# Kernel optimization log

Measured on AMD Instinct MI355X. Metric: run time of the kernel, lower is better.

Reference implementation:

```python
import jax, jax.numpy as jnp
import numpy as np

STEPS = [1, 2, 3, 4, 5]
B, N, D, H = 16, 512, 512, 8
S = len(STEPS) + 1           # identity + one stack per step
FFN_HID = 2 * S              # ffn_hidden_multiplier = 2


def setup_inputs() -> dict:
    key = jax.random.key(0)
    ks = jax.random.split(key, 12)
    h = jax.random.normal(ks[0], (B, N, D), dtype=jnp.float32)
    adj = jax.random.uniform(ks[1], (B, N, N), dtype=jnp.float32)
    mask = jax.random.randint(ks[2], (B, N), 0, 2).astype(bool)
    mask = mask.at[:, 0].set(True)  # guarantee >=1 valid node per graph
    sd = 1.0 / np.sqrt(D)
    in_proj_w = jax.random.normal(ks[3], (3 * D, D), dtype=jnp.float32) * sd
    in_proj_b = jnp.zeros((3 * D,), dtype=jnp.float32)
    out_w = jax.random.normal(ks[4], (D, D), dtype=jnp.float32) * sd
    out_b = jnp.zeros((D,), dtype=jnp.float32)
    ffn_w1 = jax.random.normal(ks[5], (S, FFN_HID), dtype=jnp.float32) * (1.0 / np.sqrt(S))
    ffn_b1 = jnp.zeros((FFN_HID,), dtype=jnp.float32)
    ffn_w2 = jax.random.normal(ks[6], (FFN_HID, H), dtype=jnp.float32) * (1.0 / np.sqrt(FFN_HID))
    ffn_b2 = jnp.zeros((H,), dtype=jnp.float32)
    return dict(h=h, adj=adj, mask=mask,
                in_proj_w=in_proj_w, in_proj_b=in_proj_b,
                out_w=out_w, out_b=out_b,
                ffn_w1=ffn_w1, ffn_b1=ffn_b1, ffn_w2=ffn_w2, ffn_b2=ffn_b2)


def _adj_stack(adj, mask):
    # Mask invalid node pairs, row-normalize to a transition matrix P,
    # then stack [I, P^s for s in STEPS] -> [B, S, N, N].
    pair_mask = mask[:, :, None] & mask[:, None, :]
    A = jnp.where(pair_mask, adj, 0.0)
    rs = A.sum(-1, keepdims=True)
    P = A / jnp.where(rs == 0.0, 1.0, rs)
    eye = jnp.broadcast_to(jnp.eye(N, dtype=adj.dtype), (adj.shape[0], N, N))
    stacks = [eye]
    pw = eye
    for step in range(1, max(STEPS) + 1):
        pw = pw @ P
        if step in STEPS:
            stacks.append(pw)
    return jnp.stack(stacks, axis=1)  # [B, S, N, N]


def reference(h, adj, mask, in_proj_w, in_proj_b, out_w, out_b,
              ffn_w1, ffn_b1, ffn_w2, ffn_b2):
    hd = D // H
    stacks = _adj_stack(adj, mask)                      # [B,S,N,N]
    # per-pair edge FFN: [B,N,N,S] -> relu -> [B,N,N,H] -> [B,H,N,N]
    edge_in = stacks.transpose(0, 2, 3, 1)
    bias = jax.nn.relu(edge_in @ ffn_w1 + ffn_b1) @ ffn_w2 + ffn_b2
    bias = bias.transpose(0, 3, 1, 2)                   # [B,H,N,N]

    qkv = h @ in_proj_w.T + in_proj_b                   # [B,N,3D]
    q, k, v = jnp.split(qkv, 3, axis=-1)
    q = q.reshape(B, N, H, hd).transpose(0, 2, 1, 3)    # [B,H,N,hd]
    k = k.reshape(B, N, H, hd).transpose(0, 2, 1, 3)
    v = v.reshape(B, N, H, hd).transpose(0, 2, 1, 3)

    scores = jnp.einsum('bhqd,bhkd->bhqk', q, k) / np.sqrt(hd) + bias
    scores = jnp.where(mask[:, None, None, :], scores, -1e9)  # key padding
    attn = jax.nn.softmax(scores, axis=-1)              # [B,H,N,N]

    ctx = jnp.einsum('bhqk,bhkd->bhqd', attn, v)
    ctx = ctx.transpose(0, 2, 1, 3).reshape(B, N, D)
    atten_out = ctx @ out_w.T + out_b                   # [B,N,D]
    atten_weights = attn.mean(axis=1)                   # [B,N,N], head-avg as in torch MHA
    return atten_out, atten_weights
```

## Files before the change

### kernel.cpp

```cpp
#include <hip/hip_runtime.h>
#include <hip/hip_bf16.h>

#define Bz 16
#define Nn 512
#define Dd 512
#define Hh 8
#define HD 64

static const long NNl  = (long)Nn * Nn;
static const long BNNl = (long)Bz * Nn * Nn;

__device__ inline float bf2f(unsigned short u) {
    unsigned int x = ((unsigned int)u) << 16;
    return __uint_as_float(x);
}
__device__ inline unsigned short f2bf(float f) {
    __hip_bfloat16 h = __float2bfloat16(f);
    return *reinterpret_cast<unsigned short*>(&h);
}

__global__ __launch_bounds__(64)
void computeP(const float* __restrict__ adj, const int* __restrict__ mask,
              float* __restrict__ P)
{
    const int i = blockIdx.x;
    const int b = blockIdx.y;
    const int lane = threadIdx.x;
    const float* arow = adj + ((long)b * Nn + i) * Nn;
    const int*   mrow = mask + (long)b * Nn;
    const bool mi = (mrow[i] != 0);

    float vals[8];
    float s = 0.f;
    #pragma unroll
    for (int t = 0; t < 2; ++t) {
        const int c = lane * 4 + t * 256;
        float4 a4 = *(const float4*)&arow[c];
        int4   m4 = *(const int4*)&mrow[c];
        float v0 = (mi && m4.x) ? a4.x : 0.f;
        float v1 = (mi && m4.y) ? a4.y : 0.f;
        float v2 = (mi && m4.z) ? a4.z : 0.f;
        float v3 = (mi && m4.w) ? a4.w : 0.f;
        vals[t*4+0] = v0; vals[t*4+1] = v1; vals[t*4+2] = v2; vals[t*4+3] = v3;
        s += v0 + v1 + v2 + v3;
    }
    #pragma unroll
    for (int o = 1; o < 64; o <<= 1) s += __shfl_xor(s, o);
    const float den = (s == 0.f) ? 1.f : s;

    float* prow = P + ((long)b * Nn + i) * Nn;
    #pragma unroll
    for (int t = 0; t < 2; ++t) {
        const int c = lane * 4 + t * 256;
        float4 o4;
        o4.x = vals[t*4+0] / den;
        o4.y = vals[t*4+1] / den;
        o4.z = vals[t*4+2] / den;
        o4.w = vals[t*4+3] / den;
        *(float4*)&prow[c] = o4;
    }
}

template<bool BT, bool BIAS>
__global__ __launch_bounds__(256)
void gemm128(const float* __restrict__ A, const float* __restrict__ Bm,
             const float* __restrict__ bias, float* __restrict__ C,
             int M, int N, int K, long sA, long sB, long sC)
{
    __shared__ float As[16][128];
    __shared__ float Bs[16][128];

    const int bz = blockIdx.z;
    A  += (long)bz * sA;
    Bm += (long)bz * sB;
    C  += (long)bz * sC;
    const int bm = blockIdx.y * 128;
    const int bn = blockIdx.x * 128;
    const int tid = threadIdx.x;
    const int tx = tid & 15;
    const int ty = tid >> 4;

    float acc[8][8];
    #pragma unroll
    for (int i = 0; i < 8; ++i)
        #pragma unroll
        for (int j = 0; j < 8; ++j) acc[i][j] = 0.f;

    for (int k0 = 0; k0 < K; k0 += 16) {
        #pragma unroll
        for (int i = 0; i < 2; ++i) {
            const int r = (tid >> 2) + i * 64;
            const int c = (tid & 3) * 4;
            float4 a4 = *(const float4*)&A[(long)(bm + r) * K + k0 + c];
            As[c+0][r] = a4.x; As[c+1][r] = a4.y;
            As[c+2][r] = a4.z; As[c+3][r] = a4.w;
        }
        if (!BT) {
            #pragma unroll
            for (int i = 0; i < 2; ++i) {
                const int kk = (tid >> 5) + i * 8;
                const int c  = (tid & 31) * 4;
                *(float4*)&Bs[kk][c] =
                    *(const float4*)&Bm[(long)(k0 + kk) * N + bn + c];
            }
        } else {
            #pragma unroll
            for (int i = 0; i < 2; ++i) {
                const int cc = (tid >> 2) + i * 64;
                const int kk = (tid & 3) * 4;
                float4 b4 = *(const float4*)&Bm[(long)(bn + cc) * K + k0 + kk];
                Bs[kk+0][cc] = b4.x; Bs[kk+1][cc] = b4.y;
                Bs[kk+2][cc] = b4.z; Bs[kk+3][cc] = b4.w;
            }
        }
        __syncthreads();

        #pragma unroll
        for (int kk = 0; kk < 16; ++kk) {
            float a[8], bb[8];
            *(float4*)&a[0]  = *(const float4*)&As[kk][ty*4];
            *(float4*)&a[4]  = *(const float4*)&As[kk][64 + ty*4];
            *(float4*)&bb[0] = *(const float4*)&Bs[kk][tx*4];
            *(float4*)&bb[4] = *(const float4*)&Bs[kk][64 + tx*4];
            #pragma unroll
            for (int i = 0; i < 8; ++i)
                #pragma unroll
                for (int j = 0; j < 8; ++j)
                    acc[i][j] = fmaf(a[i], bb[j], acc[i][j]);
        }
        __syncthreads();
    }

    float bv[8];
    if (BIAS) {
        *(float4*)&bv[0] = *(const float4*)&bias[bn + tx*4];
        *(float4*)&bv[4] = *(const float4*)&bias[bn + 64 + tx*4];
    }
    #pragma unroll
    for (int i = 0; i < 8; ++i) {
        const int r = bm + ((i < 4) ? (ty*4 + i) : (64 + ty*4 + (i - 4)));
        float o0[4], o1[4];
        #pragma unroll
        for (int j = 0; j < 4; ++j) {
            o0[j] = acc[i][j]     + (BIAS ? bv[j]     : 0.f);
            o1[j] = acc[i][j + 4] + (BIAS ? bv[j + 4] : 0.f);
        }
        *(float4*)&C[(long)r * N + bn + tx*4]      = *(float4*)o0;
        *(float4*)&C[(long)r * N + bn + 64 + tx*4] = *(float4*)o1;
    }
}

template<bool BT, bool BIAS>
__global__ __launch_bounds__(256)
void gemm64(const float* __restrict__ A, const float* __restrict__ Bm,
            const float* __restrict__ bias, float* __restrict__ C,
            int M, int N, int K, long sA, long sB, long sC)
{
    __shared__ float As[16][128];
    __shared__ float Bs[16][64];

    const int bz = blockIdx.z;
    A  += (long)bz * sA;
    Bm += (long)bz * sB;
    C  += (long)bz * sC;
    const int bm = blockIdx.y * 128;
    const int bn = blockIdx.x * 64;
    const int tid = threadIdx.x;
    const int tx = tid & 15;
    const int ty = tid >> 4;

    float acc[8][4];
    #pragma unroll
    for (int i = 0; i < 8; ++i)
        #pragma unroll
        for (int j = 0; j < 4; ++j) acc[i][j] = 0.f;

    for (int k0 = 0; k0 < K; k0 += 16) {
        #pragma unroll
        for (int i = 0; i < 2; ++i) {
            const int r = (tid >> 2) + i * 64;
            const int c = (tid & 3) * 4;
            float4 a4 = *(const float4*)&A[(long)(bm + r) * K + k0 + c];
            As[c+0][r] = a4.x; As[c+1][r] = a4.y;
            As[c+2][r] = a4.z; As[c+3][r] = a4.w;
        }
        if (!BT) {
            const int kk = tid >> 4;
            const int c  = (tid & 15) * 4;
            *(float4*)&Bs[kk][c] =
                *(const float4*)&Bm[(long)(k0 + kk) * N + bn + c];
        } else {
            const int cc = tid >> 2;
            const int kk = (tid & 3) * 4;
            float4 b4 = *(const float4*)&Bm[(long)(bn + cc) * K + k0 + kk];
            Bs[kk+0][cc] = b4.x; Bs[kk+1][cc] = b4.y;
            Bs[kk+2][cc] = b4.z; Bs[kk+3][cc] = b4.w;
        }
        __syncthreads();

        #pragma unroll
        for (int kk = 0; kk < 16; ++kk) {
            float a[8], bb[4];
            *(float4*)&a[0]  = *(const float4*)&As[kk][ty*4];
            *(float4*)&a[4]  = *(const float4*)&As[kk][64 + ty*4];
            *(float4*)&bb[0] = *(const float4*)&Bs[kk][tx*4];
            #pragma unroll
            for (int i = 0; i < 8; ++i)
                #pragma unroll
                for (int j = 0; j < 4; ++j)
                    acc[i][j] = fmaf(a[i], bb[j], acc[i][j]);
        }
        __syncthreads();
    }

    float bv[4];
    if (BIAS) *(float4*)&bv[0] = *(const float4*)&bias[bn + tx*4];
    #pragma unroll
    for (int i = 0; i < 8; ++i) {
        const int r = bm + ((i < 4) ? (ty*4 + i) : (64 + ty*4 + (i - 4)));
        float o0[4];
        #pragma unroll
        for (int j = 0; j < 4; ++j)
            o0[j] = acc[i][j] + (BIAS ? bv[j] : 0.f);
        *(float4*)&C[(long)r * N + bn + tx*4] = *(float4*)o0;
    }
}

template<bool BF16OUT>
__global__ __launch_bounds__(256)
void bias_ffn(const float* __restrict__ powers,
              const float* __restrict__ w1, const float* __restrict__ b1,
              const float* __restrict__ w2, const float* __restrict__ b2,
              void* __restrict__ biasOut)
{
    __shared__ float sw1[6][12], sb1[12], sw2[12][8], sb2[8];
    const int tid = threadIdx.x;
    if (tid < 72)        sw1[tid/12][tid%12] = w1[tid];
    else if (tid < 84)   sb1[tid-72] = b1[tid-72];
    else if (tid < 180)  sw2[(tid-84)/8][(tid-84)%8] = w2[tid-84];
    else if (tid < 188)  sb2[tid-180] = b2[tid-180];
    __syncthreads();

    const int b = blockIdx.y;
    const int ql = tid >> 7;
    const int qrow = blockIdx.x * 2 + ql;
    const int kk = (tid & 127) * 4;

    float xp[5][4];
    #pragma unroll
    for (int s = 0; s < 5; ++s) {
        float4 t = *(const float4*)&powers[((long)(s*Bz+b))*NNl + (long)qrow*Nn + kk];
        xp[s][0]=t.x; xp[s][1]=t.y; xp[s][2]=t.z; xp[s][3]=t.w;
    }
    float outh[8][4];
    #pragma unroll
    for (int j = 0; j < 4; ++j) {
        float hid[12];
        #pragma unroll
        for (int jj = 0; jj < 12; ++jj) {
            float v = sb1[jj];
            if (qrow == kk + j) v += sw1[0][jj];
            v = fmaf(xp[0][j], sw1[1][jj], v);
            v = fmaf(xp[1][j], sw1[2][jj], v);
            v = fmaf(xp[2][j], sw1[3][jj], v);
            v = fmaf(xp[3][j], sw1[4][jj], v);
            v = fmaf(xp[4][j], sw1[5][jj], v);
            hid[jj] = fmaxf(v, 0.f);
        }
        #pragma unroll
        for (int h = 0; h < 8; ++h) {
            float a = sb2[h];
            #pragma unroll
            for (int jj = 0; jj < 12; ++jj) a = fmaf(hid[jj], sw2[jj][h], a);
            outh[h][j] = a;
        }
    }
    #pragma unroll
    for (int h = 0; h < 8; ++h) {
        const long off = ((long)(b*Hh+h))*NNl + (long)qrow*Nn + kk;
        if (BF16OUT) {
            ushort4 u;
            u.x = f2bf(outh[h][0]); u.y = f2bf(outh[h][1]);
            u.z = f2bf(outh[h][2]); u.w = f2bf(outh[h][3]);
            *(ushort4*)((unsigned short*)biasOut + off) = u;
        } else {
            float4 o = {outh[h][0], outh[h][1], outh[h][2], outh[h][3]};
            *(float4*)((float*)biasOut + off) = o;
        }
    }
}

__device__ inline int kswz(int row, int slot) {
    return row * 68 + (((slot ^ ((row >> 2) & 7)) & 15) << 2);
}

template<bool BF16B>
__global__ __launch_bounds__(256)
void attn2(const float* __restrict__ qkv, const void* __restrict__ biasT,
           const int* __restrict__ mask,
           float* __restrict__ ctx, float* __restrict__ wout)
{
    __shared__ float scT[512][17];
    __shared__ float kvs[64 * 68];

    const int qt = blockIdx.x, b = blockIdx.y;
    const int q0 = qt * 16;
    const int tid = threadIdx.x;

    const int qi = tid >> 4;
    const int kg = tid & 15;
    const int kq = tid >> 6;
    const int qg = (tid >> 4) & 3;
    const int dg = tid & 15;

    float wacc[32];
    #pragma unroll
    for (int i = 0; i < 32; ++i) wacc[i] = 0.f;

    for (int h = 0; h < Hh; ++h) {
        float4 qreg[16];
        {
            const float* qp = qkv + ((long)b*Nn + q0 + qi)*(3*Dd) + h*HD;
            #pragma unroll
            for (int t = 0; t < 16; ++t) qreg[t] = *(const float4*)&qp[t*4];
        }

        for (int kt = 0; kt < 8; ++kt) {
            {
                const int row = tid >> 2;
                const int sb  = (tid & 3) * 4;
                const float* kp = qkv + ((long)b*Nn + kt*64 + row)*(3*Dd)
                                  + Dd + h*HD + sb*4;
                #pragma unroll
                for (int t = 0; t < 4; ++t)
                    *(float4*)&kvs[kswz(row, sb + t)] = *(const float4*)&kp[t*4];
            }
            __syncthreads();

            const int kbase = kt*64 + kg*4;
            const int4 m4 = *(const int4*)&mask[(long)b*Nn + kbase];
            float bias4[4];
            if (BF16B) {
                ushort4 u = *(const ushort4*)((const unsigned short*)biasT
                            + ((long)(b*Hh+h))*NNl + (long)(q0+qi)*Nn + kbase);
                bias4[0] = bf2f(u.x); bias4[1] = bf2f(u.y);
                bias4[2] = bf2f(u.z); bias4[3] = bf2f(u.w);
            } else {
                float4 f = *(const float4*)((const float*)biasT
                            + ((long)(b*Hh+h))*NNl + (long)(q0+qi)*Nn + kbase);
                bias4[0]=f.x; bias4[1]=f.y; bias4[2]=f.z; bias4[3]=f.w;
            }
            const int mm[4] = {m4.x, m4.y, m4.z, m4.w};
            #pragma unroll
            for (int j = 0; j < 4; ++j) {
                const int krow = kg*4 + j;
                float s = 0.f;
                #pragma unroll
                for (int d4 = 0; d4 < 16; ++d4) {
                    float4 k4 = *(const float4*)&kvs[kswz(krow, d4)];
                    s += qreg[d4].x*k4.x + qreg[d4].y*k4.y
                       + qreg[d4].z*k4.z + qreg[d4].w*k4.w;
                }
                float sv = s * 0.125f + bias4[j];
                if (!mm[j]) sv = -1e9f;
                scT[kbase + j][qi] = sv;
            }
            __syncthreads();
        }

        {
            const int c = kg;
            float pv[32];
            float mx = -INFINITY;
            #pragma unroll
            for (int i = 0; i < 32; ++i) {
                pv[i] = scT[c + 16*i][qi];
                mx = fmaxf(mx, pv[i]);
            }
            #pragma unroll
            for (int o = 1; o < 16; o <<= 1) mx = fmaxf(mx, __shfl_xor(mx, o));
            float sum = 0.f;
            #pragma unroll
            for (int i = 0; i < 32; ++i) { pv[i] = expf(pv[i] - mx); sum += pv[i]; }
            #pragma unroll
            for (int o = 1; o < 16; o <<= 1) sum += __shfl_xor(sum, o);
            const float inv = 1.f / sum;
            #pragma unroll
            for (int i = 0; i < 32; ++i) {
                const float p = pv[i] * inv;
                scT[c + 16*i][qi] = p;
                wacc[i] += p;
            }
        }
        __syncthreads();

        float4 acc[4];
        #pragma unroll
        for (int i = 0; i < 4; ++i) acc[i] = make_float4(0.f, 0.f, 0.f, 0.f);

        for (int kt = 0; kt < 8; ++kt) {
            {
                const int row = tid >> 2;
                const int sb  = (tid & 3) * 4;
                const float* vp = qkv + ((long)b*Nn + kt*64 + row)*(3*Dd)
                                  + 2*Dd + h*HD + sb*4;
                #pragma unroll
                for (int t = 0; t < 4; ++t)
                    *(float4*)&kvs[kswz(row, sb + t)] = *(const float4*)&vp[t*4];
            }
            __syncthreads();

            #pragma unroll
            for (int kk2 = 0; kk2 < 16; ++kk2) {
                const int kl = kq*16 + kk2;
                const int k  = kt*64 + kl;
                float p0 = scT[k][qg*4+0];
                float p1 = scT[k][qg*4+1];
                float p2 = scT[k][qg*4+2];
                float p3 = scT[k][qg*4+3];
                float4 v4 = *(const float4*)&kvs[kswz(kl, dg)];
                acc[0].x = fmaf(p0, v4.x, acc[0].x); acc[0].y = fmaf(p0, v4.y, acc[0].y);
                acc[0].z = fmaf(p0, v4.z, acc[0].z); acc[0].w = fmaf(p0, v4.w, acc[0].w);
                acc[1].x = fmaf(p1, v4.x, acc[1].x); acc[1].y = fmaf(p1, v4.y, acc[1].y);
                acc[1].z = fmaf(p1, v4.z, acc[1].z); acc[1].w = fmaf(p1, v4.w, acc[1].w);
                acc[2].x = fmaf(p2, v4.x, acc[2].x); acc[2].y = fmaf(p2, v4.y, acc[2].y);
                acc[2].z = fmaf(p2, v4.z, acc[2].z); acc[2].w = fmaf(p2, v4.w, acc[2].w);
                acc[3].x = fmaf(p3, v4.x, acc[3].x); acc[3].y = fmaf(p3, v4.y, acc[3].y);
                acc[3].z = fmaf(p3, v4.z, acc[3].z); acc[3].w = fmaf(p3, v4.w, acc[3].w);
            }
            __syncthreads();
        }

        if (kq > 0) {
            float* dst = &kvs[0] + ((long)(kq-1)*64 + (qg*16 + dg)) * 16;
            #pragma unroll
            for (int i = 0; i < 4; ++i) *(float4*)&dst[i*4] = acc[i];
        }
        __syncthreads();
        if (kq == 0) {
            #pragma unroll
            for (int k2 = 0; k2 < 3; ++k2) {
                const float* src = &kvs[0] + ((long)k2*64 + (qg*16 + dg)) * 16;
                #pragma unroll
                for (int i = 0; i < 4; ++i) {
                    float4 t = *(const float4*)&src[i*4];
                    acc[i].x += t.x; acc[i].y += t.y; acc[i].z += t.z; acc[i].w += t.w;
                }
            }
            #pragma unroll
            for (int i = 0; i < 4; ++i)
                *(float4*)&ctx[((long)b*Nn + q0 + qg*4 + i)*Dd + h*HD + dg*4] = acc[i];
        }
        __syncthreads();
    }

    {
        float* wrow = wout + ((long)b*Nn + q0 + qi) * Nn;
        #pragma unroll
        for (int i = 0; i < 32; ++i) wrow[kg + 16*i] = wacc[i] * 0.125f;
    }
}

extern "C" void kernel_launch(void* const* d_in, const int* in_sizes, int n_in,
                              void* d_out, int out_size, void* d_ws, size_t ws_size,
                              hipStream_t stream)
{
    const float* h_in      = (const float*)d_in[0];
    const float* adj       = (const float*)d_in[1];
    const int*   mask      = (const int*)d_in[2];
    const float* in_proj_w = (const float*)d_in[3];
    const float* in_proj_b = (const float*)d_in[4];
    const float* out_w     = (const float*)d_in[5];
    const float* out_b     = (const float*)d_in[6];
    const float* ffn_w1    = (const float*)d_in[7];
    const float* ffn_b1    = (const float*)d_in[8];
    const float* ffn_w2    = (const float*)d_in[9];
    const float* ffn_b2    = (const float*)d_in[10];

    float* ws = (float*)d_ws;

    float* powers = ws;
    float* qkv    = ws;
    float* ctxb   = ws + 12582912;
    void*  biasT  = (void*)((char*)d_ws + 83886080);

    const bool fp32bias = (ws_size >= 218103808ull);

    float* out_atten = (float*)d_out;
    float* out_wts   = out_atten + BNNl;

    computeP<<<dim3(Nn, Bz), 64, 0, stream>>>(adj, mask, powers);

    for (int s = 1; s < 5; ++s) {
        gemm64<false, false><<<dim3(8, 4, Bz), 256, 0, stream>>>(
            powers + (long)(s-1)*BNNl, powers, nullptr, powers + (long)s*BNNl,
            Nn, Nn, Nn, NNl, NNl, NNl);
    }

    if (fp32bias)
        bias_ffn<false><<<dim3(Nn/2, Bz), 256, 0, stream>>>(
            powers, ffn_w1, ffn_b1, ffn_w2, ffn_b2, biasT);
    else
        bias_ffn<true><<<dim3(Nn/2, Bz), 256, 0, stream>>>(
            powers, ffn_w1, ffn_b1, ffn_w2, ffn_b2, biasT);

    gemm128<true, true><<<dim3(12, 4, Bz), 256, 0, stream>>>(
        h_in, in_proj_w, in_proj_b, qkv,
        Nn, 3*Dd, Dd, (long)Nn*Dd, 0, (long)Nn*3*Dd);

    if (fp32bias)
        attn2<false><<<dim3(Nn/16, Bz), 256, 0, stream>>>(qkv, biasT, mask, ctxb, out_wts);
    else
        attn2<true><<<dim3(Nn/16, Bz), 256, 0, stream>>>(qkv, biasT, mask, ctxb, out_wts);

    gemm64<true, true><<<dim3(8, 4, Bz), 256, 0, stream>>>(
        ctxb, out_w, out_b, out_atten,
        Nn, Dd, Dd, (long)Nn*Dd, 0, (long)Nn*Dd);
}
```

Before: 961.2 us.

## Register-block two query rows per thread and stage 128-key tiles in attn2

The score phase now has each thread compute scores for two query rows against one key. This reuses every K vector read from shared memory twice, and 128 keys are staged per synchronisation instead of 64, so there are fewer barriers. The score buffer stride is padded to 20 so the P·V loop can read four probabilities with one float4 load, and the launch bounds request two blocks per CU. The costs are more registers (two 16-float4 query sets) and double the K/V shared memory. The reduction scratch stride of 17 makes its float4 LDS accesses misaligned, which could split or misbehave.

```diff
diff --git a/kernel.cpp b/kernel.cpp
--- a/kernel.cpp
+++ b/kernel.cpp
@@ -295,18 +295,23 @@
 }
 
 template<bool BF16B>
-__global__ __launch_bounds__(256)
+__global__ __launch_bounds__(256, 2)
 void attn2(const float* __restrict__ qkv, const void* __restrict__ biasT,
            const int* __restrict__ mask,
            float* __restrict__ ctx, float* __restrict__ wout)
 {
-    __shared__ float scT[512][17];
-    __shared__ float kvs[64 * 68];
+    __shared__ float scTf[512 * 20];
+    __shared__ float kvs[2 * 4352];
 
     const int qt = blockIdx.x, b = blockIdx.y;
     const int q0 = qt * 16;
     const int tid = threadIdx.x;
 
+    const int w     = tid >> 6;
+    const int lane  = tid & 63;
+    const int tsel  = w >> 1;
+    const int qbase = 8 * (w & 1) + 2 * (lane >> 4);
+    const int kgq   = lane & 15;
     const int qi = tid >> 4;
     const int kg = tid & 15;
     const int kq = tid >> 6;
@@ -318,63 +323,68 @@
     for (int i = 0; i < 32; ++i) wacc[i] = 0.f;
 
     for (int h = 0; h < Hh; ++h) {
-        float4 qreg[16];
         {
-            const float* qp = qkv + ((long)b*Nn + q0 + qi)*(3*Dd) + h*HD;
-            #pragma unroll
-            for (int t = 0; t < 16; ++t) qreg[t] = *(const float4*)&qp[t*4];
-        }
-
-        for (int kt = 0; kt < 8; ++kt) {
-            {
-                const int row = tid >> 2;
-                const int sb  = (tid & 3) * 4;
-                const float* kp = qkv + ((long)b*Nn + kt*64 + row)*(3*Dd)
-                                  + Dd + h*HD + sb*4;
+            float4 qA[16], qB[16];
+            const float* qp0 = qkv + ((long)b*Nn + q0 + qbase)*(3*Dd) + h*HD;
+            const float* qp1 = qp0 + 3*Dd;
+            #pragma unroll
+            for (int t = 0; t < 16; ++t) {
+                qA[t] = *(const float4*)&qp0[t*4];
+                qB[t] = *(const float4*)&qp1[t*4];
+            }
+
+            for (int p = 0; p < 4; ++p) {
+                {
+                    const int row  = tid >> 1;
+                    const int half = tid & 1;
+                    const float* kp = qkv + ((long)b*Nn + p*128 + row)*(3*Dd)
+                                      + Dd + h*HD + half*32;
+                    float* base = &kvs[(row >> 6) * 4352];
+                    const int rIT = row & 63;
+                    #pragma unroll
+                    for (int t = 0; t < 8; ++t)
+                        *(float4*)&base[kswz(rIT, half*8 + t)] = *(const float4*)&kp[t*4];
+                }
+                __syncthreads();
+
                 #pragma unroll
-                for (int t = 0; t < 4; ++t)
-                    *(float4*)&kvs[kswz(row, sb + t)] = *(const float4*)&kp[t*4];
-            }
-            __syncthreads();
-
-            const int kbase = kt*64 + kg*4;
-            const int4 m4 = *(const int4*)&mask[(long)b*Nn + kbase];
-            float bias4[4];
-            if (BF16B) {
-                ushort4 u = *(const ushort4*)((const unsigned short*)biasT
-                            + ((long)(b*Hh+h))*NNl + (long)(q0+qi)*Nn + kbase);
-                bias4[0] = bf2f(u.x); bias4[1] = bf2f(u.y);
-                bias4[2] = bf2f(u.z); bias4[3] = bf2f(u.w);
-            } else {
-                float4 f = *(const float4*)((const float*)biasT
-                            + ((long)(b*Hh+h))*NNl + (long)(q0+qi)*Nn + kbase);
-                bias4[0]=f.x; bias4[1]=f.y; bias4[2]=f.z; bias4[3]=f.w;
-            }
-            const int mm[4] = {m4.x, m4.y, m4.z, m4.w};
-            #pragma unroll
-            for (int j = 0; j < 4; ++j) {
-                const int krow = kg*4 + j;
-                float s = 0.f;
-                #pragma unroll
-                for (int d4 = 0; d4 < 16; ++d4) {
-                    float4 k4 = *(const float4*)&kvs[kswz(krow, d4)];
-                    s += qreg[d4].x*k4.x + qreg[d4].y*k4.y
-                       + qreg[d4].z*k4.z + qreg[d4].w*k4.w;
+                for (int j = 0; j < 4; ++j) {
+                    const int rowIT = kgq + 16*j;
+                    const float* tb = &kvs[tsel * 4352];
+                    float s0 = 0.f, s1 = 0.f;
+                    #pragma unroll
+                    for (int d4 = 0; d4 < 16; ++d4) {
+                        float4 k4 = *(const float4*)&tb[kswz(rowIT, d4)];
+                        s0 += qA[d4].x*k4.x + qA[d4].y*k4.y + qA[d4].z*k4.z + qA[d4].w*k4.w;
+                        s1 += qB[d4].x*k4.x + qB[d4].y*k4.y + qB[d4].z*k4.z + qB[d4].w*k4.w;
+                    }
+                    const int gkey = p*128 + tsel*64 + rowIT;
+                    float b0, b1;
+                    if (BF16B) {
+                        const unsigned short* bp = (const unsigned short*)biasT
+                            + ((long)(b*Hh+h))*NNl + (long)(q0+qbase)*Nn + gkey;
+                        b0 = bf2f(bp[0]); b1 = bf2f(bp[Nn]);
+                    } else {
+                        const float* bp = (const float*)biasT
+                            + ((long)(b*Hh+h))*NNl + (long)(q0+qbase)*Nn + gkey;
+                        b0 = bp[0]; b1 = bp[Nn];
+                    }
+                    const int mv = mask[(long)b*Nn + gkey];
+                    float v0 = s0 * 0.125f + b0;
+                    float v1 = s1 * 0.125f + b1;
+                    if (!mv) { v0 = -1e9f; v1 = -1e9f; }
+                    *(float2*)&scTf[gkey*20 + qbase] = make_float2(v0, v1);
                 }
-                float sv = s * 0.125f + bias4[j];
-                if (!mm[j]) sv = -1e9f;
-                scT[kbase + j][qi] = sv;
-            }
-            __syncthreads();
+                __syncthreads();
+            }
         }
 
         {
-            const int c = kg;
             float pv[32];
             float mx = -INFINITY;
             #pragma unroll
             for (int i = 0; i < 32; ++i) {
-                pv[i] = scT[c + 16*i][qi];
+                pv[i] = scTf[(kg + 16*i)*20 + qi];
                 mx = fmaxf(mx, pv[i]);
             }
             #pragma unroll
@@ -388,7 +398,7 @@
             #pragma unroll
             for (int i = 0; i < 32; ++i) {
                 const float p = pv[i] * inv;
-                scT[c + 16*i][qi] = p;
+                scTf[(kg + 16*i)*20 + qi] = p;
                 wacc[i] += p;
             }
         }
@@ -398,41 +408,45 @@
         #pragma unroll
         for (int i = 0; i < 4; ++i) acc[i] = make_float4(0.f, 0.f, 0.f, 0.f);
 
-        for (int kt = 0; kt < 8; ++kt) {
+        for (int p = 0; p < 4; ++p) {
             {
-                const int row = tid >> 2;
-                const int sb  = (tid & 3) * 4;
-                const float* vp = qkv + ((long)b*Nn + kt*64 + row)*(3*Dd)
-                                  + 2*Dd + h*HD + sb*4;
+                const int row  = tid >> 1;
+                const int half = tid & 1;
+                const float* vp = qkv + ((long)b*Nn + p*128 + row)*(3*Dd)
+                                  + 2*Dd + h*HD + half*32;
+                float* base = &kvs[(row >> 6) * 4352];
+                const int rIT = row & 63;
                 #pragma unroll
-                for (int t = 0; t < 4; ++t)
-                    *(float4*)&kvs[kswz(row, sb + t)] = *(const float4*)&vp[t*4];
+                for (int t = 0; t < 8; ++t)
+                    *(float4*)&base[kswz(rIT, half*8 + t)] = *(const float4*)&vp[t*4];
             }
             __syncthreads();
 
             #pragma unroll
-            for (int kk2 = 0; kk2 < 16; ++kk2) {
-                const int kl = kq*16 + kk2;
-                const int k  = kt*64 + kl;
-                float p0 = scT[k][qg*4+0];
-                float p1 = scT[k][qg*4+1];
-                float p2 = scT[k][qg*4+2];
-                float p3 = scT[k][qg*4+3];
-                float4 v4 = *(const float4*)&kvs[kswz(kl, dg)];
-                acc[0].x = fmaf(p0, v4.x, acc[0].x); acc[0].y = fmaf(p0, v4.y, acc[0].y);
-                acc[0].z = fmaf(p0, v4.z, acc[0].z); acc[0].w = fmaf(p0, v4.w, acc[0].w);
-                acc[1].x = fmaf(p1, v4.x, acc[1].x); acc[1].y = fmaf(p1, v4.y, acc[1].y);
-                acc[1].z = fmaf(p1, v4.z, acc[1].z); acc[1].w = fmaf(p1, v4.w, acc[1].w);
-                acc[2].x = fmaf(p2, v4.x, acc[2].x); acc[2].y = fmaf(p2, v4.y, acc[2].y);
-                acc[2].z = fmaf(p2, v4.z, acc[2].z); acc[2].w = fmaf(p2, v4.w, acc[2].w);
-                acc[3].x = fmaf(p3, v4.x, acc[3].x); acc[3].y = fmaf(p3, v4.y, acc[3].y);
-                acc[3].z = fmaf(p3, v4.z, acc[3].z); acc[3].w = fmaf(p3, v4.w, acc[3].w);
+            for (int tile = 0; tile < 2; ++tile) {
+                const float* tb = &kvs[tile * 4352];
+                const int kt = p*2 + tile;
+                #pragma unroll
+                for (int kk2 = 0; kk2 < 16; ++kk2) {
+                    const int kl = kq*16 + kk2;
+                    const int k  = kt*64 + kl;
+                    float4 p4 = *(const float4*)&scTf[k*20 + qg*4];
+                    float4 v4 = *(const float4*)&tb[kswz(kl, dg)];
+                    acc[0].x = fmaf(p4.x, v4.x, acc[0].x); acc[0].y = fmaf(p4.x, v4.y, acc[0].y);
+                    acc[0].z = fmaf(p4.x, v4.z, acc[0].z); acc[0].w = fmaf(p4.x, v4.w, acc[0].w);
+                    acc[1].x = fmaf(p4.y, v4.x, acc[1].x); acc[1].y = fmaf(p4.y, v4.y, acc[1].y);
+                    acc[1].z = fmaf(p4.y, v4.z, acc[1].z); acc[1].w = fmaf(p4.y, v4.w, acc[1].w);
+                    acc[2].x = fmaf(p4.z, v4.x, acc[2].x); acc[2].y = fmaf(p4.z, v4.y, acc[2].y);
+                    acc[2].z = fmaf(p4.z, v4.z, acc[2].z); acc[2].w = fmaf(p4.z, v4.w, acc[2].w);
+                    acc[3].x = fmaf(p4.w, v4.x, acc[3].x); acc[3].y = fmaf(p4.w, v4.y, acc[3].y);
+                    acc[3].z = fmaf(p4.w, v4.z, acc[3].z); acc[3].w = fmaf(p4.w, v4.w, acc[3].w);
+                }
             }
             __syncthreads();
         }
 
         if (kq > 0) {
-            float* dst = &kvs[0] + ((long)(kq-1)*64 + (qg*16 + dg)) * 16;
+            float* dst = &kvs[0] + ((kq-1)*64 + (qg*16 + dg)) * 17;
             #pragma unroll
             for (int i = 0; i < 4; ++i) *(float4*)&dst[i*4] = acc[i];
         }
@@ -440,7 +454,7 @@
         if (kq == 0) {
             #pragma unroll
             for (int k2 = 0; k2 < 3; ++k2) {
-                const float* src = &kvs[0] + ((long)k2*64 + (qg*16 + dg)) * 16;
+                const float* src = &kvs[0] + (k2*64 + (qg*16 + dg)) * 17;
                 #pragma unroll
                 for (int i = 0; i < 4; ++i) {
                     float4 t = *(const float4*)&src[i*4];
```

Result: no change. 975.8 us (+1.5%).
